# Optimization experiments

Measured on AMD Instinct MI355X. Metric: run time of the kernel, lower is better.

Reference implementation:

```python
import jax, jax.numpy as jnp
import numpy as np


def setup_inputs() -> dict:
    key = jax.random.key(0)
    k1, k2 = jax.random.split(key)
    BN, C, P, K = 1024, 3, 128, 15
    patches = jax.random.normal(k1, (BN, C, P, P), dtype=jnp.float32)
    kernels = jax.random.normal(k2, (BN, C, K, K), dtype=jnp.float32)
    return {
        "patches": patches,
        "kernels": kernels,
        "kernel_size": K,
        "patch_size": P,
        "fft_size": 256,  # unused by the spatial-domain path, kept for interface parity
    }


def reference(patches, kernels, kernel_size, patch_size, fft_size):
    # patches: [BN, C, P, P], kernels: [BN, C, K, K] (C == C_k branch of original)
    BN, C, P, _ = patches.shape
    K = kernel_size
    pad = K // 2
    # torch flips the kernel then runs correlation (F.conv2d) -> true convolution
    kf = jnp.flip(kernels, axis=(-2, -1))
    x = patches.reshape(1, BN * C, P, P)          # one big grouped conv
    w = kf.reshape(BN * C, 1, K, K)               # OIHW, one filter per group
    y = jax.lax.conv_general_dilated(
        x, w,
        window_strides=(1, 1),
        padding=[(pad, pad), (pad, pad)],          # zero pad == F.pad + valid conv
        dimension_numbers=("NCHW", "OIHW", "NCHW"),
        feature_group_count=BN * C,
    )
    return y.reshape(BN, C, P, P)
```

## Files before the change

kernel.cpp:

```cpp
#include <hip/hip_runtime.h>


namespace {

constexpr int P      = 128;
constexpr int K      = 15;
constexpr int HALF   = 64;
constexpr int LROWS  = HALF + K - 1;
constexpr int LM     = 36;
constexpr int LWP    = 152;
constexpr int NT     = 256;

__device__ __forceinline__ int dein(int m) {
    return (m >> 1) + (m & 1) * 20;
}

__global__ __launch_bounds__(NT, 3)
void dwconv_kernel(const float* __restrict__ patches,
                   const float* __restrict__ kernels,
                   float* __restrict__ out)
{
    __shared__ float xs[LROWS * LWP];

    const int tid   = threadIdx.x;
    const int n     = blockIdx.x >> 1;
    const int halfb = blockIdx.x & 1;
    const int ibase = halfb * HALF;

    const float* img  = patches + (size_t)n * (P * P);
    const float* kern = kernels + (size_t)n * (K * K);

    {
        int row = tid / LM;
        int m   = tid - row * LM;
        while (row < LROWS) {
            const int r  = ibase - 7 + row;
            const int g0 = m * 4 - 8;
            float4 v = make_float4(0.f, 0.f, 0.f, 0.f);
            if ((unsigned)r < (unsigned)P) {
                if (g0 >= 0 && g0 + 3 < P) {
                    v = *reinterpret_cast<const float4*>(img + r * P + g0);
                } else {
                    float t0 = 0.f, t1 = 0.f, t2 = 0.f, t3 = 0.f;
                    const float* rp = img + r * P;
                    if ((unsigned)(g0 + 0) < (unsigned)P) t0 = rp[g0 + 0];
                    if ((unsigned)(g0 + 1) < (unsigned)P) t1 = rp[g0 + 1];
                    if ((unsigned)(g0 + 2) < (unsigned)P) t2 = rp[g0 + 2];
                    if ((unsigned)(g0 + 3) < (unsigned)P) t3 = rp[g0 + 3];
                    v = make_float4(t0, t1, t2, t3);
                }
            }
            *reinterpret_cast<float4*>(xs + row * LWP + 4 * dein(m)) = v;
            row += 7; m += 4;
            if (m >= LM) { m -= LM; ++row; }
        }
    }
    __syncthreads();

    const int ty = tid >> 4;
    const int tx = tid & 15;
    const int i0 = ty * 4;
    const int j0 = tx * 8;

    const float* xbase = xs + i0 * LWP + 4 * tx;

    float acc[4][8];
    #pragma unroll
    for (int rr = 0; rr < 4; ++rr)
        #pragma unroll
        for (int s = 0; s < 8; ++s)
            acc[rr][s] = 0.0f;

    float xwA[24], xwB[24];
    float kr[4][K];

#define LOADX(W, t) do {                                                     \
        const float* xr_ = xbase + (t) * LWP;                                \
        const float4 v0_ = *reinterpret_cast<const float4*>(xr_ + 0);        \
        const float4 v1_ = *reinterpret_cast<const float4*>(xr_ + 80);       \
        const float4 v2_ = *reinterpret_cast<const float4*>(xr_ + 4);        \
        const float4 v3_ = *reinterpret_cast<const float4*>(xr_ + 84);       \
        const float4 v4_ = *reinterpret_cast<const float4*>(xr_ + 8);        \
        const float4 v5_ = *reinterpret_cast<const float4*>(xr_ + 88);       \
        W[0]=v0_.x;  W[1]=v0_.y;  W[2]=v0_.z;  W[3]=v0_.w;                   \
        W[4]=v1_.x;  W[5]=v1_.y;  W[6]=v1_.z;  W[7]=v1_.w;                   \
        W[8]=v2_.x;  W[9]=v2_.y;  W[10]=v2_.z; W[11]=v2_.w;                  \
        W[12]=v3_.x; W[13]=v3_.y; W[14]=v3_.z; W[15]=v3_.w;                  \
        W[16]=v4_.x; W[17]=v4_.y; W[18]=v4_.z; W[19]=v4_.w;                  \
        W[20]=v5_.x; W[21]=v5_.y; W[22]=v5_.z; W[23]=v5_.w;                  \
    } while (0)

#define FMAROW(W, rr, slot) do {                                             \
        _Pragma("unroll")                                                    \
        for (int b_ = 0; b_ < K; ++b_)                                       \
            _Pragma("unroll")                                                \
            for (int s_ = 0; s_ < 8; ++s_)                                   \
                acc[rr][s_] = fmaf(W[s_ + 15 - b_], kr[slot][b_],            \
                                   acc[rr][s_]);                             \
    } while (0)

    auto loadk = [&](int slot, int a) {
        #pragma unroll
        for (int b = 0; b < K; ++b) kr[slot][b] = kern[a * K + b];
    };

    loadk(2, 14); loadk(1, 13); loadk(0, 12);
    LOADX(xwA, 0);
    LOADX(xwB, 1);
    FMAROW(xwA, 0, 2);
    LOADX(xwA, 2);
    FMAROW(xwB, 0, 1); FMAROW(xwB, 1, 2);
    LOADX(xwB, 3);
    FMAROW(xwA, 0, 0); FMAROW(xwA, 1, 1); FMAROW(xwA, 2, 2);

    #pragma unroll 1
    for (int tb = 3; tb <= 11; tb += 4) {
        loadk(3, 14 - tb); LOADX(xwA, tb + 1);
        FMAROW(xwB, 1, 0); FMAROW(xwB, 2, 1); FMAROW(xwB, 3, 2);
        FMAROW(xwB, 0, 3);
        loadk(2, 13 - tb); LOADX(xwB, tb + 2);
        FMAROW(xwA, 1, 3); FMAROW(xwA, 2, 0); FMAROW(xwA, 3, 1);
        FMAROW(xwA, 0, 2);
        loadk(1, 12 - tb); LOADX(xwA, tb + 3);
        FMAROW(xwB, 1, 2); FMAROW(xwB, 2, 3); FMAROW(xwB, 3, 0);
        FMAROW(xwB, 0, 1);
        loadk(0, 11 - tb); LOADX(xwB, tb + 4);
        FMAROW(xwA, 1, 1); FMAROW(xwA, 2, 2); FMAROW(xwA, 3, 3);
        FMAROW(xwA, 0, 0);
    }

    LOADX(xwA, 16);
    FMAROW(xwB, 1, 0); FMAROW(xwB, 2, 1); FMAROW(xwB, 3, 2);
    LOADX(xwB, 17);
    FMAROW(xwA, 2, 0); FMAROW(xwA, 3, 1);
    FMAROW(xwB, 3, 0);

#undef LOADX
#undef FMAROW

    float* orow = out + (size_t)n * (P * P) + (size_t)(ibase + i0) * P + j0;
    #pragma unroll
    for (int rr = 0; rr < 4; ++rr) {
        *reinterpret_cast<float4*>(orow + rr * P + 0) =
            make_float4(acc[rr][0], acc[rr][1], acc[rr][2], acc[rr][3]);
        *reinterpret_cast<float4*>(orow + rr * P + 4) =
            make_float4(acc[rr][4], acc[rr][5], acc[rr][6], acc[rr][7]);
    }
}

}

extern "C" void kernel_launch(void* const* d_in, const int* in_sizes, int n_in,
                              void* d_out, int out_size, void* d_ws, size_t ws_size,
                              hipStream_t stream) {
    const float* patches = (const float*)d_in[0];
    const float* kernels = (const float*)d_in[1];
    float* out = (float*)d_out;

    const int n_images = in_sizes[0] / (P * P);
    const int grid = n_images * 2;

    dwconv_kernel<<<grid, NT, 0, stream>>>(patches, kernels, out);
}
```

Baseline: 504.5 us.

## Split each image into quarter-row blocks with 2-row register tiles and XOR-swizzled LDS

Each block now covers 32 output rows instead of 64, so the grid has four blocks per image, and each thread computes 2 rows by 8 columns instead of 4 by 8. Only two kernel-row register slots are kept, which frees registers and allows raising launch bounds to 5 blocks per CU. The shared-memory row stride grows to 160 and column groups are XOR-swizzled by row to reduce LDS bank conflicts. In exchange, each LDS input row is reused by fewer output rows per thread, and the halo overhead rises from 78 loaded rows per 64 outputs to 46 per 32.

```diff
diff --git a/kernel.cpp b/kernel.cpp
--- a/kernel.cpp
+++ b/kernel.cpp
@@ -5,17 +5,21 @@
 
 constexpr int P      = 128;
 constexpr int K      = 15;
-constexpr int HALF   = 64;
+constexpr int HALF   = 32;
 constexpr int LROWS  = HALF + K - 1;
 constexpr int LM     = 36;
-constexpr int LWP    = 152;
+constexpr int LWP    = 160;
 constexpr int NT     = 256;
 
 __device__ __forceinline__ int dein(int m) {
     return (m >> 1) + (m & 1) * 20;
 }
 
-__global__ __launch_bounds__(NT, 3)
+__device__ __forceinline__ int rowkey(int row) {
+    return (row >> 1) & 6;
+}
+
+__global__ __launch_bounds__(NT, 5)
 void dwconv_kernel(const float* __restrict__ patches,
                    const float* __restrict__ kernels,
                    float* __restrict__ out)
@@ -23,9 +27,9 @@
     __shared__ float xs[LROWS * LWP];
 
     const int tid   = threadIdx.x;
-    const int n     = blockIdx.x >> 1;
-    const int halfb = blockIdx.x & 1;
-    const int ibase = halfb * HALF;
+    const int n     = blockIdx.x >> 2;
+    const int qb    = blockIdx.x & 3;
+    const int ibase = qb * HALF;
 
     const float* img  = patches + (size_t)n * (P * P);
     const float* kern = kernels + (size_t)n * (K * K);
@@ -50,7 +54,7 @@
                     v = make_float4(t0, t1, t2, t3);
                 }
             }
-            *reinterpret_cast<float4*>(xs + row * LWP + 4 * dein(m)) = v;
+            *reinterpret_cast<float4*>(xs + row * LWP + 4 * (dein(m) ^ rowkey(row))) = v;
             row += 7; m += 4;
             if (m >= LM) { m -= LM; ++row; }
         }
@@ -59,88 +63,69 @@
 
     const int ty = tid >> 4;
     const int tx = tid & 15;
-    const int i0 = ty * 4;
+    const int i0 = ty * 2;
     const int j0 = tx * 8;
 
-    const float* xbase = xs + i0 * LWP + 4 * tx;
+    const int dbase[6] = { tx + 0, tx + 20, tx + 1, tx + 21, tx + 2, tx + 22 };
 
-    float acc[4][8];
+    float acc[2][8];
     #pragma unroll
-    for (int rr = 0; rr < 4; ++rr)
+    for (int rr = 0; rr < 2; ++rr)
         #pragma unroll
         for (int s = 0; s < 8; ++s)
             acc[rr][s] = 0.0f;
 
     float xwA[24], xwB[24];
-    float kr[4][K];
+    float kr0[K], kr1[K];
 
 #define LOADX(W, t) do {                                                     \
-        const float* xr_ = xbase + (t) * LWP;                                \
-        const float4 v0_ = *reinterpret_cast<const float4*>(xr_ + 0);        \
-        const float4 v1_ = *reinterpret_cast<const float4*>(xr_ + 80);       \
-        const float4 v2_ = *reinterpret_cast<const float4*>(xr_ + 4);        \
-        const float4 v3_ = *reinterpret_cast<const float4*>(xr_ + 84);       \
-        const float4 v4_ = *reinterpret_cast<const float4*>(xr_ + 8);        \
-        const float4 v5_ = *reinterpret_cast<const float4*>(xr_ + 88);       \
-        W[0]=v0_.x;  W[1]=v0_.y;  W[2]=v0_.z;  W[3]=v0_.w;                   \
-        W[4]=v1_.x;  W[5]=v1_.y;  W[6]=v1_.z;  W[7]=v1_.w;                   \
-        W[8]=v2_.x;  W[9]=v2_.y;  W[10]=v2_.z; W[11]=v2_.w;                  \
-        W[12]=v3_.x; W[13]=v3_.y; W[14]=v3_.z; W[15]=v3_.w;                  \
-        W[16]=v4_.x; W[17]=v4_.y; W[18]=v4_.z; W[19]=v4_.w;                  \
-        W[20]=v5_.x; W[21]=v5_.y; W[22]=v5_.z; W[23]=v5_.w;                  \
+        const int    lrow_ = i0 + (t);                                       \
+        const float* xr_   = xs + lrow_ * LWP;                               \
+        const int    key_  = (lrow_ >> 1) & 6;                               \
+        _Pragma("unroll")                                                    \
+        for (int q_ = 0; q_ < 6; ++q_) {                                     \
+            const float4 v_ =                                                \
+                *reinterpret_cast<const float4*>(xr_ + 4 * (dbase[q_] ^ key_)); \
+            W[q_ * 4 + 0] = v_.x; W[q_ * 4 + 1] = v_.y;                      \
+            W[q_ * 4 + 2] = v_.z; W[q_ * 4 + 3] = v_.w;                      \
+        }                                                                    \
     } while (0)
 
-#define FMAROW(W, rr, slot) do {                                             \
+#define FMAROW(W, rr, KR) do {                                               \
         _Pragma("unroll")                                                    \
         for (int b_ = 0; b_ < K; ++b_)                                       \
             _Pragma("unroll")                                                \
             for (int s_ = 0; s_ < 8; ++s_)                                   \
-                acc[rr][s_] = fmaf(W[s_ + 15 - b_], kr[slot][b_],            \
-                                   acc[rr][s_]);                             \
+                acc[rr][s_] = fmaf(W[s_ + 15 - b_], KR[b_], acc[rr][s_]);    \
     } while (0)
 
-    auto loadk = [&](int slot, int a) {
+    auto loadk = [&](float (&kr)[K], int a) {
         #pragma unroll
-        for (int b = 0; b < K; ++b) kr[slot][b] = kern[a * K + b];
+        for (int b = 0; b < K; ++b) kr[b] = kern[a * K + b];
     };
 
-    loadk(2, 14); loadk(1, 13); loadk(0, 12);
     LOADX(xwA, 0);
+    loadk(kr0, 14);
     LOADX(xwB, 1);
-    FMAROW(xwA, 0, 2);
-    LOADX(xwA, 2);
-    FMAROW(xwB, 0, 1); FMAROW(xwB, 1, 2);
-    LOADX(xwB, 3);
-    FMAROW(xwA, 0, 0); FMAROW(xwA, 1, 1); FMAROW(xwA, 2, 2);
+    FMAROW(xwA, 0, kr0);
 
     #pragma unroll 1
-    for (int tb = 3; tb <= 11; tb += 4) {
-        loadk(3, 14 - tb); LOADX(xwA, tb + 1);
-        FMAROW(xwB, 1, 0); FMAROW(xwB, 2, 1); FMAROW(xwB, 3, 2);
-        FMAROW(xwB, 0, 3);
-        loadk(2, 13 - tb); LOADX(xwB, tb + 2);
-        FMAROW(xwA, 1, 3); FMAROW(xwA, 2, 0); FMAROW(xwA, 3, 1);
-        FMAROW(xwA, 0, 2);
-        loadk(1, 12 - tb); LOADX(xwA, tb + 3);
-        FMAROW(xwB, 1, 2); FMAROW(xwB, 2, 3); FMAROW(xwB, 3, 0);
-        FMAROW(xwB, 0, 1);
-        loadk(0, 11 - tb); LOADX(xwB, tb + 4);
-        FMAROW(xwA, 1, 1); FMAROW(xwA, 2, 2); FMAROW(xwA, 3, 3);
-        FMAROW(xwA, 0, 0);
+    for (int ttb = 1; ttb <= 13; ttb += 2) {
+        loadk(kr1, 14 - ttb); LOADX(xwA, ttb + 1);
+        FMAROW(xwB, 1, kr0);
+        FMAROW(xwB, 0, kr1);
+        loadk(kr0, 13 - ttb); LOADX(xwB, ttb + 2);
+        FMAROW(xwA, 1, kr1);
+        FMAROW(xwA, 0, kr0);
     }
-
-    LOADX(xwA, 16);
-    FMAROW(xwB, 1, 0); FMAROW(xwB, 2, 1); FMAROW(xwB, 3, 2);
-    LOADX(xwB, 17);
-    FMAROW(xwA, 2, 0); FMAROW(xwA, 3, 1);
-    FMAROW(xwB, 3, 0);
+    FMAROW(xwB, 1, kr0);
 
 #undef LOADX
 #undef FMAROW
 
     float* orow = out + (size_t)n * (P * P) + (size_t)(ibase + i0) * P + j0;
     #pragma unroll
-    for (int rr = 0; rr < 4; ++rr) {
+    for (int rr = 0; rr < 2; ++rr) {
         *reinterpret_cast<float4*>(orow + rr * P + 0) =
             make_float4(acc[rr][0], acc[rr][1], acc[rr][2], acc[rr][3]);
         *reinterpret_cast<float4*>(orow + rr * P + 4) =
@@ -158,7 +143,7 @@
     float* out = (float*)d_out;
 
     const int n_images = in_sizes[0] / (P * P);
-    const int grid = n_images * 2;
+    const int grid = n_images * 4;
 
     dwconv_kernel<<<grid, NT, 0, stream>>>(patches, kernels, out);
 }
```

Result: no change. 498.0 us (-1.3%).
